# Optimization experiments

Hardware: AMD Instinct MI355X
Metric: run time of the kernel (lower is better)

Reference implementation:

```python
import jax, jax.numpy as jnp
import numpy as np

B, SEG, MEM, D, E, H = 4, 1024, 1024, 128, 128, 8  # model_dim == embed_dim required by module
TOTAL = SEG + MEM


def sinusoid_pos(length, e):
    # Transformer-XL relative sinusoid table, then flipped so row 0 = largest distance
    p = jnp.arange(length, dtype=jnp.float32)[:, None]
    j = jnp.arange(e, dtype=jnp.float32)[None, :]
    ang = p / jnp.power(jnp.float32(10000.0), 2.0 * j / e)
    enc = jnp.where((jnp.arange(e) % 2 == 0)[None, :], jnp.sin(ang), jnp.cos(ang))
    return enc[::-1]


def circulant_shift(b, shift):
    # b: (B, H, S, W). Row i of the index matrix is the rolled arange shifted by (shift - i).
    W = b.shape[-1]
    S = b.shape[-2]
    idx = jnp.roll(jnp.arange(W), shift)[::-1]
    idx2 = jnp.concatenate([idx, idx])
    win = idx2[jnp.arange(S)[:, None] + jnp.arange(W)[None, :]][:, ::-1]  # (S, W)
    return jnp.take_along_axis(b, win[None, None, :, :], axis=3)


def setup_inputs() -> dict:
    key = jax.random.key(0)
    ks = jax.random.split(key, 11)
    w = 0.02  # small init for linear weights (Linear default-ish scale)
    return {
        "x": jax.random.normal(ks[0], (B, SEG, D), dtype=jnp.float32),
        "mem": jax.random.normal(ks[1], (B, MEM, D), dtype=jnp.float32),
        "att_mask": jnp.zeros((SEG, TOTAL), dtype=bool),  # unused by the module's forward
        "u1": jax.random.normal(ks[2], (H, 1, E), dtype=jnp.float32),
        "u2": jax.random.normal(ks[3], (H, 1, E), dtype=jnp.float32),
        "w_q": jax.random.normal(ks[4], (D, H * E), dtype=jnp.float32) * w,
        "w_kv": jax.random.normal(ks[5], (D, 2 * H * E), dtype=jnp.float32) * w,
        "w_r": jax.random.normal(ks[6], (D, H * E), dtype=jnp.float32) * w,
        "w_mlp": jax.random.normal(ks[7], (H * E, D), dtype=jnp.float32) * w,
        "ln_g": jnp.ones((D,), dtype=jnp.float32),
        "ln_b": jnp.zeros((D,), dtype=jnp.float32),
    }


def reference(x, mem, att_mask, u1, u2, w_q, w_kv, w_r, w_mlp, ln_g, ln_b):
    bsz, seg, d = x.shape
    h = jnp.concatenate((mem, x), axis=1)          # (B, total, D)
    total = h.shape[1]
    mem_len = total - seg

    # NB: the original uses .view without transpose -> plain row-major reshape
    q = (x @ w_q).reshape(bsz, -1, seg, d)          # (B, H, S, E)
    kv = (h @ w_kv).reshape(2 * bsz, -1, total, d)  # (2B, H, T, E)
    k, v = kv[:bsz], kv[bsz:]

    pos = sinusoid_pos(total, d)                    # buffer pos[-total:]
    r = (pos @ w_r).reshape(-1, total, d)           # (H, T, E)

    b = jnp.einsum('bhse,hte->bhst', q, r)
    b = circulant_shift(b, -seg + 1)

    qk = jnp.einsum('bhse,bhte->bhst', q, k)
    u1k = jnp.einsum('he,bhte->bht', u1[:, 0], k)[:, :, None, :]
    u2r = jnp.einsum('he,hte->ht', u2[:, 0], r)[None, :, None, :]

    score = qk + b + u1k + u2r                      # (B, H, S, T)
    tri = (jnp.arange(total)[None, :] - jnp.arange(seg)[:, None]) <= mem_len
    score = jnp.where(tri[None, None], score, 0.0) / jnp.sqrt(jnp.float32(d))
    score = jnp.where(score == 0.0, -jnp.inf, score)  # faithful zeros->-inf trick
    score = jax.nn.softmax(score, axis=-1)

    att = jnp.einsum('bhst,bhte->bhse', score, v).reshape(bsz, seg, -1)
    y = att @ w_mlp + x
    mu = jnp.mean(y, axis=-1, keepdims=True)
    var = jnp.mean((y - mu) ** 2, axis=-1, keepdims=True)
    return (y - mu) / jnp.sqrt(var + 1e-5) * ln_g + ln_b
```

## Files before the change

### kernel.cpp

```cpp
#include <hip/hip_runtime.h>
#include <hip/hip_bf16.h>
#include <stdint.h>

typedef __bf16 bf16;
typedef __attribute__((ext_vector_type(8))) __bf16 bf16x8;
typedef __attribute__((ext_vector_type(4))) __bf16 bf16x4;
typedef __attribute__((ext_vector_type(4))) float f32x4;

#define KSC 0.12764932952880681f

__device__ __forceinline__ f32x4 MFMA(bf16x8 a, bf16x8 b, f32x4 c) {
  return __builtin_amdgcn_mfma_f32_16x16x32_bf16(a, b, c, 0, 0, 0);
}

__device__ __forceinline__ void GLL16(const void* g, void* l) {
  __builtin_amdgcn_global_load_lds(
      (const __attribute__((address_space(1))) void*)g,
      (__attribute__((address_space(3))) void*)l, 16, 0, 0);
}

__device__ __forceinline__ bf16 tobf(float f) { return (bf16)f; }

__global__ __launch_bounds__(256) void k_prep(
    const float* __restrict__ x, const float* __restrict__ mm,
    const float* __restrict__ wq, const float* __restrict__ wkv,
    const float* __restrict__ wr, const float* __restrict__ wmlp,
    bf16* __restrict__ posb, bf16* __restrict__ wq_bt, bf16* __restrict__ wkv_bt,
    bf16* __restrict__ wr_bt, bf16* __restrict__ wmlp_bt,
    bf16* __restrict__ xb, bf16* __restrict__ memb)
{
  __shared__ float T[32][33];
  const int b = blockIdx.x;
  const int tid = threadIdx.x;
  if (b < 1024) {
    int id = b * 256 + tid;
    int t = id >> 7, j = id & 127;
    float p = (float)(2047 - t);
    float ang = p * exp2f(-(float)j * 0.20762050593046264f);
    float v = ((j & 1) == 0) ? __sinf(ang) : __cosf(ang);
    posb[id] = tobf(v);
    return;
  }
  if (b < 1664) {
    int tb = b - 1024;
    const float* src; bf16* dst; int R, C, r0, c0;
    if (tb < 128)      { src = wq;   dst = wq_bt;   R = 128;  C = 1024; r0 = (tb >> 5) * 32;        c0 = (tb & 31) * 32; }
    else if (tb < 384) { int t2 = tb - 128; src = wkv;  dst = wkv_bt;  R = 128;  C = 2048; r0 = (t2 >> 6) * 32; c0 = (t2 & 63) * 32; }
    else if (tb < 512) { int t2 = tb - 384; src = wr;   dst = wr_bt;   R = 128;  C = 1024; r0 = (t2 >> 5) * 32; c0 = (t2 & 31) * 32; }
    else               { int t2 = tb - 512; src = wmlp; dst = wmlp_bt; R = 1024; C = 128;  r0 = (t2 >> 2) * 32; c0 = (t2 & 3) * 32; }
    int r = tid >> 3, c4 = (tid & 7) * 4;
    f32x4 v = *(const f32x4*)(src + (size_t)(r0 + r) * C + c0 + c4);
    T[r][c4] = v[0]; T[r][c4 + 1] = v[1]; T[r][c4 + 2] = v[2]; T[r][c4 + 3] = v[3];
    __syncthreads();
    bf16x4 o;
#pragma unroll
    for (int k = 0; k < 4; ++k) o[k] = tobf(T[c4 + k][r]);
    *(bf16x4*)(dst + (size_t)(c0 + r) * R + r0 + c4) = o;
    return;
  }
  {
    int cb = b - 1664;
    if (cb < 512) {
      int i = cb * 256 + tid;
      f32x4 v = *(const f32x4*)(x + (size_t)i * 4);
      bf16x4 o; o[0]=tobf(v[0]); o[1]=tobf(v[1]); o[2]=tobf(v[2]); o[3]=tobf(v[3]);
      *(bf16x4*)(xb + (size_t)i * 4) = o;
    } else {
      int i = (cb - 512) * 256 + tid;
      f32x4 v = *(const f32x4*)(mm + (size_t)i * 4);
      bf16x4 o; o[0]=tobf(v[0]); o[1]=tobf(v[1]); o[2]=tobf(v[2]); o[3]=tobf(v[3]);
      *(bf16x4*)(memb + (size_t)i * 4) = o;
    }
  }
}

template <int MODE>
__global__ __launch_bounds__(256, 2) void k_proj(
    const bf16* __restrict__ asrc, const bf16* __restrict__ asrc2,
    const bf16* __restrict__ wbt, bf16* __restrict__ out0, bf16* __restrict__ out1,
    const float* __restrict__ u1, const float* __restrict__ u2)
{
  __shared__ bf16 As[64 * 128];
  __shared__ bf16 Bs[128 * 128];
  const int m0 = blockIdx.x * 64;
  const int n0 = blockIdx.y * 128;
  const int tid = threadIdx.x;
  const int w = tid >> 6, lane = tid & 63, g = lane >> 4, c = lane & 15;

#pragma unroll
  for (int it = 0; it < 4; ++it) {
    int ch = w * 256 + it * 64 + lane;
    int row = ch >> 4, cc = ch & 15;
    int scc = cc ^ (row & 7);
    const bf16* src;
    if (MODE == 1) {
      int rg = m0 + row;
      int bb = rg >> 11, t = rg & 2047;
      src = (t < 1024) ? (asrc2 + (size_t)(bb * 1024 + t) * 128)
                       : (asrc + (size_t)(bb * 1024 + (t - 1024)) * 128);
    } else {
      src = asrc + (size_t)(m0 + row) * 128;
    }
    GLL16(src + scc * 8, (char*)As + (w * 256 + it * 64) * 16);
  }
#pragma unroll
  for (int it = 0; it < 8; ++it) {
    int ch = w * 512 + it * 64 + lane;
    int n = ch >> 4, cc = ch & 15;
    int scc = cc ^ (n & 7);
    GLL16(wbt + (size_t)(n0 + n) * 128 + scc * 8, (char*)Bs + (w * 512 + it * 64) * 16);
  }
  __syncthreads();

  f32x4 acc[8] = {};
#pragma unroll
  for (int kk = 0; kk < 4; ++kk) {
    bf16x8 a = *(const bf16x8*)((const char*)As + (16 * w + c) * 256 + (((4 * kk + g) ^ (c & 7)) << 4));
#pragma unroll
    for (int fo = 0; fo < 8; ++fo) {
      bf16x8 b = *(const bf16x8*)((const char*)Bs + (16 * fo + c) * 256 + (((4 * kk + g) ^ (c & 7)) << 4));
      acc[fo] = MFMA(a, b, acc[fo]);
    }
  }

#pragma unroll
  for (int fo = 0; fo < 8; ++fo) {
#pragma unroll
    for (int j = 0; j < 4; ++j) {
      int rg = m0 + 16 * w + 4 * g + j;
      int cg = n0 + 16 * fo + c;
      float av = acc[fo][j];
      if (MODE == 0) {
        int b = rg >> 10, s2 = rg & 1023;
        int nn = s2 >> 7;
        int s = ((s2 & 127) << 3) | (cg >> 7);
        int e = cg & 127;
        size_t idx = ((size_t)((b * 8 + nn) * 1024 + s)) * 128 + e;
        out0[idx] = tobf((av + u1[nn * 128 + e]) * KSC);
        out1[idx] = tobf((av + u2[nn * 128 + e]) * KSC);
      } else if (MODE == 1) {
        int bb = rg >> 11, t = rg & 2047;
        int nn = (t >> 7) & 7;
        int hlf = (t >> 10) & 1;
        int t2 = ((t & 127) << 4) | (cg >> 7);
        int e = cg & 127;
        bf16 v = tobf(av);
        if (bb < 2)
          out0[((size_t)(((2 * bb + hlf) * 8 + nn) * 2048 + t2)) * 128 + e] = v;
        else
          out1[((size_t)(((2 * (bb - 2) + hlf) * 8 + nn) * 2048 + t2)) * 128 + e] = v;
      } else {
        int nn = rg >> 8;
        int t = ((rg & 255) << 3) | (cg >> 7);
        int e = cg & 127;
        bf16 v = tobf(av);
        out0[((size_t)(nn * 2112 + t)) * 128 + e] = v;
        if (t < 64) out0[((size_t)(nn * 2112 + 2048 + t)) * 128 + e] = v;
      }
    }
  }
}

__global__ __launch_bounds__(256) void k_vtrans(const bf16* __restrict__ vh, bf16* __restrict__ vht)
{
  __shared__ bf16 T[64][72];
  int bt = blockIdx.x * 64, be = blockIdx.y * 64, bh = blockIdx.z;
  const bf16* src = vh + (size_t)bh * 2048 * 128;
  bf16* dst = vht + (size_t)bh * 128 * 2048;
#pragma unroll
  for (int i2 = 0; i2 < 2; ++i2) {
    int ch = i2 * 256 + threadIdx.x;
    int tt = ch >> 3, cc = ch & 7;
    bf16x8 v = *(const bf16x8*)(src + (size_t)(bt + tt) * 128 + be + cc * 8);
    *(bf16x8*)&T[tt][cc * 8] = v;
  }
  __syncthreads();
#pragma unroll
  for (int i2 = 0; i2 < 2; ++i2) {
    int ch = i2 * 256 + threadIdx.x;
    int ee = ch >> 3, c2 = ch & 7;
    bf16x8 o;
#pragma unroll
    for (int m = 0; m < 8; ++m) o[m] = T[c2 * 8 + m][ee];
    *(bf16x8*)(dst + (size_t)(be + ee) * 2048 + bt + c2 * 8) = o;
  }
}

__global__ __launch_bounds__(256, 2) void k_flash(
    const bf16* __restrict__ qhk, const bf16* __restrict__ qhr,
    const bf16* __restrict__ kh, const bf16* __restrict__ vht,
    const bf16* __restrict__ rhe, bf16* __restrict__ att2)
{
  __shared__ bf16 Ks[2][64 * 128];
  __shared__ bf16 Vs[2][64 * 128];
  __shared__ char QRS[4][2688];

  const int x = blockIdx.x;
  const int xcd = x & 7;
  const int k2 = x >> 3;
  const int bh = 8 * (k2 & 3) + xcd;
  const int qb = (k2 < 32) ? (k2 >> 2) : (23 - (k2 >> 2));
  const int ib = bh >> 3, nh = bh & 7;
  const int s0 = qb * 64;
  const int tid = threadIdx.x;
  const int w = tid >> 6, lane = tid & 63, g = lane >> 4, c = lane & 15;

  const bf16* qkb  = qhk + (size_t)bh * 1024 * 128;
  const bf16* qrb  = qhr + (size_t)bh * 1024 * 128;
  const bf16* kbase = kh + (size_t)bh * 2048 * 128;
  const bf16* vbase = vht + (size_t)bh * 128 * 2048;
  const bf16* rbase = rhe + (size_t)nh * 2112 * 128;

  const int nt = qb + 17;

  const bf16 *kp0, *kp1, *vp0, *vp1, *vp2, *vp3;
  {
    int ch0 = w * 256 + lane;
    int ch1 = ch0 + 64;
    int r0 = ch0 >> 4, cc0 = ch0 & 15;
    int r1 = ch1 >> 4, cc1 = ch1 & 15;
    kp0 = kbase + (size_t)r0 * 128 + (cc0 ^ (r0 & 7)) * 8;
    kp1 = kbase + (size_t)r1 * 128 + (cc1 ^ (r1 & 7)) * 8;
    int e0 = ch0 >> 3, t0c = ch0 & 7;
    int e1 = ch1 >> 3, t1c = ch1 & 7;
    int e2 = e0 + 16, e3 = e1 + 16;
    vp0 = vbase + (size_t)e0 * 2048 + (t0c ^ (e0 & 7)) * 8;
    vp1 = vbase + (size_t)e1 * 2048 + (t1c ^ (e1 & 7)) * 8;
    vp2 = vbase + (size_t)e2 * 2048 + (t0c ^ (e2 & 7)) * 8;
    vp3 = vbase + (size_t)e3 * 2048 + (t1c ^ (e3 & 7)) * 8;
  }
  const int dof = (w * 256 + lane) * 16;

  auto stage = [&](int pb) {
    char* Kd = (char*)Ks[pb];
    char* Vd = (char*)Vs[pb];
    GLL16(kp0, Kd + dof);
    GLL16(kp1, Kd + dof + 1024);
    GLL16(kp0 + 1024, Kd + dof + 2048);
    GLL16(kp1 + 1024, Kd + dof + 3072);
    GLL16(vp0, Vd + dof);
    GLL16(vp1, Vd + dof + 1024);
    GLL16(vp2, Vd + dof + 2048);
    GLL16(vp3, Vd + dof + 3072);
    kp0 += 8192; kp1 += 8192;
    vp0 += 64; vp1 += 64; vp2 += 64; vp3 += 64;
  };

  bf16x8 qfK[4], qfR[4];
  {
    int srow = s0 + 16 * w + c;
#pragma unroll
    for (int kk = 0; kk < 4; ++kk) {
      qfK[kk] = *(const bf16x8*)(qkb + (size_t)srow * 128 + kk * 32 + g * 8);
      qfR[kk] = *(const bf16x8*)(qrb + (size_t)srow * 128 + kk * 32 + g * 8);
    }
  }

  bf16x8 rf[5][4];
  const bf16* rp[5];
  {
    const int L0 = 1008 - s0 - 16 * w + c;
#pragma unroll
    for (int f2 = 0; f2 < 5; ++f2) {
      rp[f2] = rbase + (size_t)(L0 + 16 * f2) * 128 + g * 8;
#pragma unroll
      for (int kk = 0; kk < 4; ++kk) rf[f2][kk] = *(const bf16x8*)(rp[f2] + kk * 32);
      rp[f2] += 64 * 128;
    }
  }

  f32x4 Ot[8] = {};
  float m_r = -1e30f, l_r = 0.f;

  stage(0);

  for (int tt = 0; tt < nt; ++tt) {
    __syncthreads();
    const bool notlast = (tt + 1 < nt);
    if (notlast) stage((tt + 1) & 1);

    const bf16* Kc = Ks[tt & 1];
    const bf16* Vc = Vs[tt & 1];

    f32x4 sacc[4] = {};
    __builtin_amdgcn_s_setprio(1);
#pragma unroll
    for (int kk = 0; kk < 4; ++kk) {
#pragma unroll
      for (int f = 0; f < 4; ++f) {
        bf16x8 kf = *(const bf16x8*)((const char*)Kc + (16 * f + c) * 256 + (((4 * kk + g) ^ (c & 7)) << 4));
        sacc[f] = MFMA(kf, qfK[kk], sacc[f]);
      }
    }
    f32x4 bacc[5] = {};
#pragma unroll
    for (int f2 = 0; f2 < 5; ++f2)
#pragma unroll
      for (int kk = 0; kk < 4; ++kk)
        bacc[f2] = MFMA(rf[f2][kk], qfR[kk], bacc[f2]);
    __builtin_amdgcn_s_setprio(0);

    bf16* qrw = (bf16*)QRS[w];
#pragma unroll
    for (int f2 = 0; f2 < 5; ++f2)
#pragma unroll
      for (int j = 0; j < 4; ++j)
        qrw[c * 82 + 16 * f2 + 4 * g + j] = tobf(bacc[f2][j]);

    if (notlast) {
#pragma unroll
      for (int f2 = 0; f2 < 5; ++f2) {
#pragma unroll
        for (int kk = 0; kk < 4; ++kk) rf[f2][kk] = *(const bf16x8*)(rp[f2] + kk * 32);
        rp[f2] += 64 * 128;
      }
    }

    float zv[4][4];
#pragma unroll
    for (int f = 0; f < 4; ++f)
#pragma unroll
      for (int j = 0; j < 4; ++j) {
        int tl = 16 * f + 4 * g + j;
        float z = sacc[f][j] + (float)qrw[c * 82 + (tl - c + 15)];
        if (!notlast && (tl > 16 * w + c)) z = -1e30f;
        zv[f][j] = z;
      }

    float pm = fmaxf(fmaxf(fmaxf(zv[0][0], zv[0][1]), fmaxf(zv[0][2], zv[0][3])),
                     fmaxf(fmaxf(zv[1][0], zv[1][1]), fmaxf(zv[1][2], zv[1][3])));
    float pm2 = fmaxf(fmaxf(fmaxf(zv[2][0], zv[2][1]), fmaxf(zv[2][2], zv[2][3])),
                      fmaxf(fmaxf(zv[3][0], zv[3][1]), fmaxf(zv[3][2], zv[3][3])));
    pm = fmaxf(pm, pm2);
    pm = fmaxf(pm, __shfl_xor(pm, 16));
    pm = fmaxf(pm, __shfl_xor(pm, 32));

    float alpha = 1.f;
    if (!__all(pm <= m_r + 8.0f)) {
      float mn = fmaxf(m_r, pm);
      alpha = exp2f(m_r - mn);
      m_r = mn;
      float at[4];
#pragma unroll
      for (int j = 0; j < 4; ++j) at[j] = __shfl(alpha, 20 * g + j);
#pragma unroll
      for (int fo = 0; fo < 8; ++fo)
#pragma unroll
        for (int j = 0; j < 4; ++j) Ot[fo][j] *= at[j];
    }

    float ps = 0.f;
#pragma unroll
    for (int f = 0; f < 4; ++f)
#pragma unroll
      for (int j = 0; j < 4; ++j) { float pp = exp2f(zv[f][j] - m_r); zv[f][j] = pp; ps += pp; }
    ps += __shfl_xor(ps, 16);
    ps += __shfl_xor(ps, 32);
    l_r = l_r * alpha + ps;

    bf16* pw = (bf16*)QRS[w];
#pragma unroll
    for (int f = 0; f < 4; ++f)
#pragma unroll
      for (int j = 0; j < 4; ++j) {
        int t = 16 * f + 4 * g + j;
        pw[c * 80 + ((((t >> 3) ^ (c & 7)) << 3) | (t & 7))] = tobf(zv[f][j]);
      }

    __builtin_amdgcn_s_setprio(1);
#pragma unroll
    for (int kk2 = 0; kk2 < 2; ++kk2) {
      bf16x8 pa = *(const bf16x8*)(pw + c * 80 + (((4 * kk2 + g) ^ (c & 7)) << 3));
#pragma unroll
      for (int fo = 0; fo < 8; ++fo) {
        int e = 16 * fo + c;
        bf16x8 vf = *(const bf16x8*)((const char*)Vc + e * 128 + (((4 * kk2 + g) ^ (c & 7)) << 4));
        Ot[fo] = MFMA(pa, vf, Ot[fo]);
      }
    }
    __builtin_amdgcn_s_setprio(0);
  }

  float linv[4];
#pragma unroll
  for (int j = 0; j < 4; ++j) linv[j] = 1.f / __shfl(l_r, 20 * g + j);
  bf16* ob = att2 + (size_t)ib * 1024 * 1024;
#pragma unroll
  for (int j = 0; j < 4; ++j) {
    int sg = s0 + 16 * w + 4 * g + j;
    size_t rowb = (size_t)(nh * 128 + (sg >> 3)) * 1024 + ((sg & 7) << 7);
#pragma unroll
    for (int fo = 0; fo < 8; ++fo)
      ob[rowb + 16 * fo + c] = tobf(Ot[fo][j] * linv[j]);
  }
}

__global__ __launch_bounds__(256, 2) void k_mlp(
    const bf16* __restrict__ att2, const bf16* __restrict__ wmlp_bt,
    const float* __restrict__ x, const float* __restrict__ lng, const float* __restrict__ lnb,
    float* __restrict__ out)
{
  __shared__ bf16 As[64 * 128];
  __shared__ bf16 Bs[128 * 128];
  const int m0 = blockIdx.x * 64;
  const int tid = threadIdx.x;
  const int w = tid >> 6, lane = tid & 63, g = lane >> 4, c = lane & 15;

  f32x4 acc[8] = {};
  for (int ks = 0; ks < 8; ++ks) {
    int k0 = ks * 128;
    __syncthreads();
#pragma unroll
    for (int it = 0; it < 4; ++it) {
      int ch = w * 256 + it * 64 + lane;
      int row = ch >> 4, cc = ch & 15;
      GLL16(att2 + (size_t)(m0 + row) * 1024 + k0 + ((cc ^ (row & 7)) * 8),
            (char*)As + (w * 256 + it * 64) * 16);
    }
#pragma unroll
    for (int it = 0; it < 8; ++it) {
      int ch = w * 512 + it * 64 + lane;
      int n = ch >> 4, cc = ch & 15;
      GLL16(wmlp_bt + (size_t)n * 1024 + k0 + ((cc ^ (n & 7)) * 8),
            (char*)Bs + (w * 512 + it * 64) * 16);
    }
    __syncthreads();
#pragma unroll
    for (int kk = 0; kk < 4; ++kk) {
      bf16x8 a = *(const bf16x8*)((const char*)As + (16 * w + c) * 256 + (((4 * kk + g) ^ (c & 7)) << 4));
#pragma unroll
      for (int fo = 0; fo < 8; ++fo) {
        bf16x8 b = *(const bf16x8*)((const char*)Bs + (16 * fo + c) * 256 + (((4 * kk + g) ^ (c & 7)) << 4));
        acc[fo] = MFMA(a, b, acc[fo]);
      }
    }
  }
#pragma unroll
  for (int j = 0; j < 4; ++j) {
    int rg = m0 + 16 * w + 4 * g + j;
    float y[8];
    float s1 = 0.f, s2 = 0.f;
#pragma unroll
    for (int fo = 0; fo < 8; ++fo) {
      float v = acc[fo][j] + x[(size_t)rg * 128 + 16 * fo + c];
      y[fo] = v; s1 += v; s2 += v * v;
    }
#pragma unroll
    for (int d = 1; d < 16; d <<= 1) { s1 += __shfl_xor(s1, d); s2 += __shfl_xor(s2, d); }
    float mu = s1 * 0.0078125f;
    float var = s2 * 0.0078125f - mu * mu;
    float rs = rsqrtf(var + 1e-5f);
#pragma unroll
    for (int fo = 0; fo < 8; ++fo) {
      int e = 16 * fo + c;
      out[(size_t)rg * 128 + e] = (y[fo] - mu) * rs * lng[e] + lnb[e];
    }
  }
}

extern "C" void kernel_launch(void* const* d_in, const int* in_sizes, int n_in,
                              void* d_out, int out_size, void* d_ws, size_t ws_size,
                              hipStream_t stream)
{
  const float* x    = (const float*)d_in[0];
  const float* mm   = (const float*)d_in[1];
  const float* u1   = (const float*)d_in[3];
  const float* u2   = (const float*)d_in[4];
  const float* wq   = (const float*)d_in[5];
  const float* wkv  = (const float*)d_in[6];
  const float* wr   = (const float*)d_in[7];
  const float* wmlp = (const float*)d_in[8];
  const float* lng  = (const float*)d_in[9];
  const float* lnb  = (const float*)d_in[10];
  float* out = (float*)d_out;

  char* p = (char*)d_ws;
  bf16* posb    = (bf16*)p;  p += (size_t)262144 * 2;
  bf16* wq_bt   = (bf16*)p;  p += (size_t)131072 * 2;
  bf16* wkv_bt  = (bf16*)p;  p += (size_t)262144 * 2;
  bf16* wr_bt   = (bf16*)p;  p += (size_t)131072 * 2;
  bf16* wmlp_bt = (bf16*)p;  p += (size_t)131072 * 2;
  bf16* xb      = (bf16*)p;  p += (size_t)524288 * 2;
  bf16* memb    = (bf16*)p;  p += (size_t)524288 * 2;
  bf16* qhk     = (bf16*)p;  p += (size_t)4 * 8 * 1024 * 128 * 2;
  bf16* qhr     = (bf16*)p;  p += (size_t)4 * 8 * 1024 * 128 * 2;
  bf16* kh      = (bf16*)p;  p += (size_t)4 * 8 * 2048 * 128 * 2;
  bf16* vh      = (bf16*)p;  p += (size_t)4 * 8 * 2048 * 128 * 2;
  bf16* vht     = (bf16*)p;  p += (size_t)4 * 8 * 2048 * 128 * 2;
  bf16* rhe     = (bf16*)p;  p += (size_t)8 * 2112 * 128 * 2;
  bf16* att2    = (bf16*)p;  p += (size_t)4 * 1024 * 1024 * 2;

  k_prep<<<dim3(2688), dim3(256), 0, stream>>>(x, mm, wq, wkv, wr, wmlp,
                                               posb, wq_bt, wkv_bt, wr_bt, wmlp_bt, xb, memb);
  k_proj<0><<<dim3(64, 8),   dim3(256), 0, stream>>>(xb,  (const bf16*)nullptr, wq_bt,  qhk, qhr, u1, u2);
  k_proj<1><<<dim3(128, 16), dim3(256), 0, stream>>>(xb,  memb,                 wkv_bt, kh,  vh,  nullptr, nullptr);
  k_proj<2><<<dim3(32, 8),   dim3(256), 0, stream>>>(posb,(const bf16*)nullptr, wr_bt,  rhe, (bf16*)nullptr, nullptr, nullptr);
  k_vtrans<<<dim3(32, 2, 32), dim3(256), 0, stream>>>(vh, vht);
  k_flash<<<dim3(512), dim3(256), 0, stream>>>(qhk, qhr, kh, vht, rhe, att2);
  k_mlp<<<dim3(64), dim3(256), 0, stream>>>(att2, wmlp_bt, x, lng, lnb, out);
}
```

Baseline: 269.9 us.

## Load K fragments into registers and software-pipeline PV behind next tile's QK

In the flash kernel, K tiles are now read straight from global memory into registers and prefetched one tile ahead, so K no longer goes through LDS. The P·V product is deferred by one iteration using a double-buffered per-wave P buffer, letting it overlap the next tile's QK and positional-bias MFMAs, with a single barrier per iteration. The bias and P stores are vectorised into bf16x4 writes. The MLP kernel double-buffers its A/B LDS tiles and drops to one block per SM, trading occupancy and more registers for load/compute overlap.

```diff
diff --git a/kernel.cpp b/kernel.cpp
--- a/kernel.cpp
+++ b/kernel.cpp
@@ -191,9 +191,9 @@
     const bf16* __restrict__ kh, const bf16* __restrict__ vht,
     const bf16* __restrict__ rhe, bf16* __restrict__ att2)
 {
-  __shared__ bf16 Ks[2][64 * 128];
   __shared__ bf16 Vs[2][64 * 128];
-  __shared__ char QRS[4][2688];
+  __shared__ bf16 QRS[4][16 * 84];
+  __shared__ bf16 Ps[4][2][16 * 80];
 
   const int x = blockIdx.x;
   const int xcd = x & 7;
@@ -207,20 +207,15 @@
 
   const bf16* qkb  = qhk + (size_t)bh * 1024 * 128;
   const bf16* qrb  = qhr + (size_t)bh * 1024 * 128;
-  const bf16* kbase = kh + (size_t)bh * 2048 * 128;
   const bf16* vbase = vht + (size_t)bh * 128 * 2048;
   const bf16* rbase = rhe + (size_t)nh * 2112 * 128;
 
   const int nt = qb + 17;
 
-  const bf16 *kp0, *kp1, *vp0, *vp1, *vp2, *vp3;
+  const bf16 *vp0, *vp1, *vp2, *vp3;
   {
     int ch0 = w * 256 + lane;
     int ch1 = ch0 + 64;
-    int r0 = ch0 >> 4, cc0 = ch0 & 15;
-    int r1 = ch1 >> 4, cc1 = ch1 & 15;
-    kp0 = kbase + (size_t)r0 * 128 + (cc0 ^ (r0 & 7)) * 8;
-    kp1 = kbase + (size_t)r1 * 128 + (cc1 ^ (r1 & 7)) * 8;
     int e0 = ch0 >> 3, t0c = ch0 & 7;
     int e1 = ch1 >> 3, t1c = ch1 & 7;
     int e2 = e0 + 16, e3 = e1 + 16;
@@ -231,18 +226,12 @@
   }
   const int dof = (w * 256 + lane) * 16;
 
-  auto stage = [&](int pb) {
-    char* Kd = (char*)Ks[pb];
+  auto stageV = [&](int pb) {
     char* Vd = (char*)Vs[pb];
-    GLL16(kp0, Kd + dof);
-    GLL16(kp1, Kd + dof + 1024);
-    GLL16(kp0 + 1024, Kd + dof + 2048);
-    GLL16(kp1 + 1024, Kd + dof + 3072);
     GLL16(vp0, Vd + dof);
     GLL16(vp1, Vd + dof + 1024);
     GLL16(vp2, Vd + dof + 2048);
     GLL16(vp3, Vd + dof + 3072);
-    kp0 += 8192; kp1 += 8192;
     vp0 += 64; vp1 += 64; vp2 += 64; vp3 += 64;
   };
 
@@ -255,6 +244,14 @@
       qfR[kk] = *(const bf16x8*)(qrb + (size_t)srow * 128 + kk * 32 + g * 8);
     }
   }
+
+  const bf16* kfb = kh + (size_t)bh * 2048 * 128 + (size_t)c * 128 + g * 8;
+  bf16x8 kf[4][4];
+#pragma unroll
+  for (int kk = 0; kk < 4; ++kk)
+#pragma unroll
+    for (int f = 0; f < 4; ++f)
+      kf[kk][f] = *(const bf16x8*)(kfb + f * 2048 + kk * 32);
 
   bf16x8 rf[5][4];
   const bf16* rp[5];
@@ -272,49 +269,68 @@
   f32x4 Ot[8] = {};
   float m_r = -1e30f, l_r = 0.f;
 
-  stage(0);
+  stageV(0);
+  __syncthreads();
 
   for (int tt = 0; tt < nt; ++tt) {
-    __syncthreads();
     const bool notlast = (tt + 1 < nt);
-    if (notlast) stage((tt + 1) & 1);
-
-    const bf16* Kc = Ks[tt & 1];
-    const bf16* Vc = Vs[tt & 1];
 
     f32x4 sacc[4] = {};
     __builtin_amdgcn_s_setprio(1);
 #pragma unroll
-    for (int kk = 0; kk < 4; ++kk) {
-#pragma unroll
-      for (int f = 0; f < 4; ++f) {
-        bf16x8 kf = *(const bf16x8*)((const char*)Kc + (16 * f + c) * 256 + (((4 * kk + g) ^ (c & 7)) << 4));
-        sacc[f] = MFMA(kf, qfK[kk], sacc[f]);
-      }
-    }
-    f32x4 bacc[5] = {};
-#pragma unroll
-    for (int f2 = 0; f2 < 5; ++f2)
+    for (int kk = 0; kk < 4; ++kk)
+#pragma unroll
+      for (int f = 0; f < 4; ++f)
+        sacc[f] = MFMA(kf[kk][f], qfK[kk], sacc[f]);
+    __builtin_amdgcn_s_setprio(0);
+
+    if (notlast) {
+      kfb += 8192;
 #pragma unroll
       for (int kk = 0; kk < 4; ++kk)
-        bacc[f2] = MFMA(rf[f2][kk], qfR[kk], bacc[f2]);
-    __builtin_amdgcn_s_setprio(0);
-
-    bf16* qrw = (bf16*)QRS[w];
-#pragma unroll
-    for (int f2 = 0; f2 < 5; ++f2)
-#pragma unroll
-      for (int j = 0; j < 4; ++j)
-        qrw[c * 82 + 16 * f2 + 4 * g + j] = tobf(bacc[f2][j]);
-
-    if (notlast) {
-#pragma unroll
-      for (int f2 = 0; f2 < 5; ++f2) {
+#pragma unroll
+        for (int f = 0; f < 4; ++f)
+          kf[kk][f] = *(const bf16x8*)(kfb + f * 2048 + kk * 32);
+    }
+
+    bf16* qrw = &QRS[w][0];
+    __builtin_amdgcn_s_setprio(1);
+#pragma unroll
+    for (int f2 = 0; f2 < 5; ++f2) {
+      f32x4 bacc = {};
+#pragma unroll
+      for (int kk = 0; kk < 4; ++kk) bacc = MFMA(rf[f2][kk], qfR[kk], bacc);
+      bf16x4 pk;
+#pragma unroll
+      for (int j = 0; j < 4; ++j) pk[j] = tobf(bacc[j]);
+      *(bf16x4*)(qrw + c * 84 + 16 * f2 + 4 * g) = pk;
+      if (notlast) {
 #pragma unroll
         for (int kk = 0; kk < 4; ++kk) rf[f2][kk] = *(const bf16x8*)(rp[f2] + kk * 32);
         rp[f2] += 64 * 128;
       }
     }
+    __builtin_amdgcn_s_setprio(0);
+
+    if (tt > 0) {
+      const bf16* Vc = Vs[(tt - 1) & 1];
+      const bf16* pp = &Ps[w][(tt - 1) & 1][0];
+      __builtin_amdgcn_s_setprio(1);
+#pragma unroll
+      for (int kk2 = 0; kk2 < 2; ++kk2) {
+        bf16x8 pa = *(const bf16x8*)(pp + c * 80 + (((4 * kk2 + g) ^ (c & 7)) << 3));
+#pragma unroll
+        for (int fo = 0; fo < 8; ++fo) {
+          int e = 16 * fo + c;
+          bf16x8 vf = *(const bf16x8*)((const char*)Vc + e * 128 + (((4 * kk2 + g) ^ (c & 7)) << 4));
+          Ot[fo] = MFMA(pa, vf, Ot[fo]);
+        }
+      }
+      __builtin_amdgcn_s_setprio(0);
+    }
+
+    __syncthreads();
+    if (notlast) stageV((tt + 1) & 1);
 
     float zv[4][4];
 #pragma unroll
@@ -322,7 +338,7 @@
 #pragma unroll
       for (int j = 0; j < 4; ++j) {
         int tl = 16 * f + 4 * g + j;
-        float z = sacc[f][j] + (float)qrw[c * 82 + (tl - c + 15)];
+        float z = sacc[f][j] + (float)qrw[c * 84 + (tl - c + 15)];
         if (!notlast && (tl > 16 * w + c)) z = -1e30f;
         zv[f][j] = z;
       }
@@ -353,24 +369,29 @@
 #pragma unroll
     for (int f = 0; f < 4; ++f)
 #pragma unroll
-      for (int j = 0; j < 4; ++j) { float pp = exp2f(zv[f][j] - m_r); zv[f][j] = pp; ps += pp; }
+      for (int j = 0; j < 4; ++j) { float pp2 = exp2f(zv[f][j] - m_r); zv[f][j] = pp2; ps += pp2; }
     ps += __shfl_xor(ps, 16);
     ps += __shfl_xor(ps, 32);
     l_r = l_r * alpha + ps;
 
-    bf16* pw = (bf16*)QRS[w];
-#pragma unroll
-    for (int f = 0; f < 4; ++f)
-#pragma unroll
-      for (int j = 0; j < 4; ++j) {
-        int t = 16 * f + 4 * g + j;
-        pw[c * 80 + ((((t >> 3) ^ (c & 7)) << 3) | (t & 7))] = tobf(zv[f][j]);
-      }
-
-    __builtin_amdgcn_s_setprio(1);
+    {
+      bf16* pp = &Ps[w][tt & 1][0];
+#pragma unroll
+      for (int f = 0; f < 4; ++f) {
+        bf16x4 pk;
+#pragma unroll
+        for (int j = 0; j < 4; ++j) pk[j] = tobf(zv[f][j]);
+        *(bf16x4*)(pp + c * 80 + ((((2 * f + (g >> 1)) ^ (c & 7)) << 3) | (4 * g & 7))) = pk;
+      }
+    }
+  }
+
+  {
+    const bf16* Vc = Vs[(nt - 1) & 1];
+    const bf16* pp = &Ps[w][(nt - 1) & 1][0];
 #pragma unroll
     for (int kk2 = 0; kk2 < 2; ++kk2) {
-      bf16x8 pa = *(const bf16x8*)(pw + c * 80 + (((4 * kk2 + g) ^ (c & 7)) << 3));
+      bf16x8 pa = *(const bf16x8*)(pp + c * 80 + (((4 * kk2 + g) ^ (c & 7)) << 3));
 #pragma unroll
       for (int fo = 0; fo < 8; ++fo) {
         int e = 16 * fo + c;
@@ -378,7 +399,6 @@
         Ot[fo] = MFMA(pa, vf, Ot[fo]);
       }
     }
-    __builtin_amdgcn_s_setprio(0);
   }
 
   float linv[4];
@@ -395,42 +415,48 @@
   }
 }
 
-__global__ __launch_bounds__(256, 2) void k_mlp(
+__global__ __launch_bounds__(256, 1) void k_mlp(
     const bf16* __restrict__ att2, const bf16* __restrict__ wmlp_bt,
     const float* __restrict__ x, const float* __restrict__ lng, const float* __restrict__ lnb,
     float* __restrict__ out)
 {
-  __shared__ bf16 As[64 * 128];
-  __shared__ bf16 Bs[128 * 128];
+  __shared__ bf16 As[2][64 * 128];
+  __shared__ bf16 Bs[2][128 * 128];
   const int m0 = blockIdx.x * 64;
   const int tid = threadIdx.x;
   const int w = tid >> 6, lane = tid & 63, g = lane >> 4, c = lane & 15;
 
-  f32x4 acc[8] = {};
-  for (int ks = 0; ks < 8; ++ks) {
+  auto stage = [&](int ks, int pb) {
     int k0 = ks * 128;
-    __syncthreads();
 #pragma unroll
     for (int it = 0; it < 4; ++it) {
       int ch = w * 256 + it * 64 + lane;
       int row = ch >> 4, cc = ch & 15;
       GLL16(att2 + (size_t)(m0 + row) * 1024 + k0 + ((cc ^ (row & 7)) * 8),
-            (char*)As + (w * 256 + it * 64) * 16);
+            (char*)As[pb] + (w * 256 + it * 64) * 16);
     }
 #pragma unroll
     for (int it = 0; it < 8; ++it) {
       int ch = w * 512 + it * 64 + lane;
       int n = ch >> 4, cc = ch & 15;
       GLL16(wmlp_bt + (size_t)n * 1024 + k0 + ((cc ^ (n & 7)) * 8),
-            (char*)Bs + (w * 512 + it * 64) * 16);
-    }
+            (char*)Bs[pb] + (w * 512 + it * 64) * 16);
+    }
+  };
+
+  f32x4 acc[8] = {};
+  stage(0, 0);
+  for (int ks = 0; ks < 8; ++ks) {
     __syncthreads();
+    if (ks + 1 < 8) stage(ks + 1, (ks + 1) & 1);
+    const char* Ac = (const char*)As[ks & 1];
+    const char* Bc = (const char*)Bs[ks & 1];
 #pragma unroll
     for (int kk = 0; kk < 4; ++kk) {
-      bf16x8 a = *(const bf16x8*)((const char*)As + (16 * w + c) * 256 + (((4 * kk + g) ^ (c & 7)) << 4));
+      bf16x8 a = *(const bf16x8*)(Ac + (16 * w + c) * 256 + (((4 * kk + g) ^ (c & 7)) << 4));
 #pragma unroll
       for (int fo = 0; fo < 8; ++fo) {
-        bf16x8 b = *(const bf16x8*)((const char*)Bs + (16 * fo + c) * 256 + (((4 * kk + g) ^ (c & 7)) << 4));
+        bf16x8 b = *(const bf16x8*)(Bc + (16 * fo + c) * 256 + (((4 * kk + g) ^ (c & 7)) << 4));
         acc[fo] = MFMA(a, b, acc[fo]);
       }
     }
```

New measurement: 416.4 us. 54.2% more time.
